# Optimization experiments

Measured on AMD Instinct MI355X. Metric: run time of the kernel, lower is better.

## Reference

```python
import jax, jax.numpy as jnp
import numpy as np

B, S_ENC, S_DEC = 4, 2048, 1024
ENC_DIM, DEC_DIM, H = 1024, 1024, 16
CROSS_DIM = max(ENC_DIM, DEC_DIM)
HEAD_DIM_DEC = DEC_DIM // H
SCALE = HEAD_DIM_DEC ** 0.5  # module divides by dec_scaling only


def _linear_params(key, d_in, d_out):
    kw, kb = jax.random.split(key)
    bound = 1.0 / np.sqrt(d_in)
    W = jax.random.uniform(kw, (d_in, d_out), jnp.float32, -bound, bound)
    b = jax.random.uniform(kb, (d_out,), jnp.float32, -bound, bound)
    return W, b


def setup_inputs() -> dict:
    key = jax.random.key(0)
    ks = jax.random.split(key, 7)
    enc = jax.random.normal(ks[0], (B, S_ENC, ENC_DIM), jnp.float32)
    dec = jax.random.normal(ks[1], (B, S_DEC, DEC_DIM), jnp.float32)
    enc_mask = jax.random.uniform(ks[2], (B, 1, 1, S_ENC)) < 0.1
    q_w, q_b = _linear_params(ks[3], DEC_DIM, CROSS_DIM)
    k_w, k_b = _linear_params(ks[4], ENC_DIM, CROSS_DIM)
    v_w, v_b = _linear_params(ks[5], ENC_DIM, DEC_DIM)
    o_w, o_b = _linear_params(ks[6], DEC_DIM, DEC_DIM)
    return {"enc": enc, "enc_mask": enc_mask, "dec": dec,
            "q_w": q_w, "q_b": q_b, "k_w": k_w, "k_b": k_b,
            "v_w": v_w, "v_b": v_b, "o_w": o_w, "o_b": o_b}


def _split_heads(x):
    b, s, d = x.shape
    return x.reshape(b, s, H, d // H).transpose(0, 2, 1, 3)  # [b,h,s,hd]


def reference(enc, enc_mask, dec, q_w, q_b, k_w, k_b, v_w, v_b, o_w, o_b):
    q = _split_heads(dec @ q_w + q_b)   # [B,H,Sq,cross_hd]
    k = _split_heads(enc @ k_w + k_b)   # [B,H,Sk,cross_hd]
    v = _split_heads(enc @ v_w + v_b)   # [B,H,Sk,dec_hd]
    logits = jnp.einsum('bhqd,bhkd->bhqk', q, k) / SCALE
    logits = jnp.where(enc_mask, -jnp.inf, logits)
    a = jax.nn.softmax(logits, axis=-1)
    x = jnp.einsum('bhqk,bhkd->bhqd', a, v)          # [B,H,Sq,dec_hd]
    x = x.transpose(0, 2, 1, 3).reshape(x.shape[0], x.shape[2], -1)  # [B,Sq,DEC_DIM]
    return x @ o_w + o_b
```

## Files before the change

kernel.cpp:

```cpp
#include <hip/hip_runtime.h>
#include <hip/hip_bf16.h>
#include <cstdint>

#define BB   4
#define SENC 2048
#define SDEC 1024
#define DM   1024
#define NH   16
#define HD   64

using short8 = __attribute__((ext_vector_type(8))) short;
using f32x4  = __attribute__((ext_vector_type(4))) float;

__device__ inline unsigned short f2bf(float f) {
    return (unsigned short)((__builtin_bit_cast(unsigned int, f) + 0x8000u) >> 16);
}
__device__ inline unsigned int pk2bf(float a, float b) {
    return ((__builtin_bit_cast(unsigned int, a) + 0x8000u) >> 16) |
           ((__builtin_bit_cast(unsigned int, b) + 0x8000u) & 0xffff0000u);
}

__device__ inline float fexp2(float x) {
#if __has_builtin(__builtin_amdgcn_exp2f)
    return __builtin_amdgcn_exp2f(x);
#else
    return exp2f(x);
#endif
}

#if __has_builtin(__builtin_amdgcn_global_load_lds)
#define HAS_GLL 1
#endif

__device__ inline void stage16(const void* g, void* l) {
#ifdef HAS_GLL
    typedef __attribute__((address_space(1))) const unsigned int guint;
    typedef __attribute__((address_space(3))) unsigned int luint;
    __builtin_amdgcn_global_load_lds((guint*)g, (luint*)l, 16, 0, 0);
#else
    *(short8*)l = *(const short8*)g;
#endif
}

__global__ __launch_bounds__(256) void cvt2_kernel(const float* __restrict__ dec,
                                                   const float* __restrict__ enc,
                                                   unsigned short* __restrict__ out) {
    const int nd = BB * SDEC * DM;
    int i = (blockIdx.x * 256 + threadIdx.x) * 4;
    const float* src = (i < nd) ? (dec + i) : (enc + (i - nd));
    float4 v = *(const float4*)src;
    ushort4 o;
    o.x = f2bf(v.x); o.y = f2bf(v.y); o.z = f2bf(v.z); o.w = f2bf(v.w);
    *(ushort4*)(out + i) = o;
}

__global__ __launch_bounds__(256) void wtrans_kernel(
    const float* __restrict__ qw, const float* __restrict__ kw,
    const float* __restrict__ vw, const float* __restrict__ ow,
    unsigned short* __restrict__ qwt, unsigned short* __restrict__ kvwt,
    unsigned short* __restrict__ owt) {
    const float* src; unsigned short* dst;
    switch (blockIdx.z) {
        case 0:  src = qw; dst = qwt; break;
        case 1:  src = kw; dst = kvwt; break;
        case 2:  src = vw; dst = kvwt + (size_t)1024 * DM; break;
        default: src = ow; dst = owt; break;
    }
    __shared__ float t[64][65];
    const int k0 = blockIdx.y * 64, n0 = blockIdx.x * 64;
    const int tid = threadIdx.x;
    #pragma unroll
    for (int it = 0; it < 16; ++it) {
        int e = it * 256 + tid, r = e >> 6, c = e & 63;
        t[r][c] = src[(size_t)(k0 + r) * DM + n0 + c];
    }
    __syncthreads();
    #pragma unroll
    for (int it = 0; it < 16; ++it) {
        int e = it * 256 + tid, r = e >> 6, c = e & 63;
        dst[(size_t)(n0 + r) * DM + k0 + c] = f2bf(t[c][r]);
    }
}

__global__ __launch_bounds__(256) void gemm_qkv_kernel(
    const unsigned short* __restrict__ encb, const unsigned short* __restrict__ decb,
    const unsigned short* __restrict__ kvwt, const unsigned short* __restrict__ qwt,
    const float* __restrict__ q_b, const float* __restrict__ k_b, const float* __restrict__ v_b,
    unsigned short* __restrict__ Qb, unsigned short* __restrict__ Kb,
    unsigned short* __restrict__ Vtb) {
    __shared__ __align__(16) unsigned short As[128 * 32];
    __shared__ __align__(16) unsigned short Bs[128 * 32];
    const int id = blockIdx.x;
    const bool isKV = id < 1024;
    const unsigned short *A, *Bt;
    int m0, n0;
    if (isKV) { A = encb; Bt = kvwt; m0 = (id >> 4) * 128; n0 = (id & 15) * 128; }
    else      { int i2 = id - 1024; A = decb; Bt = qwt; m0 = (i2 >> 3) * 128; n0 = (i2 & 7) * 128; }
    const int tid = threadIdx.x;
    const int wave = tid >> 6, lane = tid & 63, quad = lane >> 4, l16 = lane & 15;
    const int wr = wave >> 1, wc = wave & 1;
    const int r16 = lane >> 2, c8 = (lane & 3) * 8;
    f32x4 acc[4][4] = {};
    for (int kb = 0; kb < DM; kb += 32) {
        #pragma unroll
        for (int i = 0; i < 2; ++i) {
            const int row = wave * 32 + i * 16 + r16;
            stage16(&A[(size_t)(m0 + row) * DM + kb + c8], &As[row * 32 + c8]);
            stage16(&Bt[(size_t)(n0 + row) * DM + kb + c8], &Bs[row * 32 + c8]);
        }
        __syncthreads();
        short8 af[4], bfr[4];
        #pragma unroll
        for (int i = 0; i < 4; ++i) af[i] = *(const short8*)&As[(wr * 64 + i * 16 + l16) * 32 + quad * 8];
        #pragma unroll
        for (int j = 0; j < 4; ++j) bfr[j] = *(const short8*)&Bs[(wc * 64 + j * 16 + l16) * 32 + quad * 8];
        #pragma unroll
        for (int i = 0; i < 4; ++i)
            #pragma unroll
            for (int j = 0; j < 4; ++j)
                acc[i][j] = __builtin_amdgcn_mfma_f32_16x16x32_bf16(af[i], bfr[j], acc[i][j], 0, 0, 0);
        __syncthreads();
    }
    #pragma unroll
    for (int i = 0; i < 4; ++i) {
        #pragma unroll
        for (int j = 0; j < 4; ++j) {
            const int gc = n0 + wc * 64 + j * 16 + l16;
            #pragma unroll
            for (int rr = 0; rr < 4; ++rr) {
                const int gr = m0 + wr * 64 + i * 16 + quad * 4 + rr;
                if (!isKV) {
                    int b = gr >> 10, sq = gr & 1023, h = gc >> 6, d = gc & 63;
                    float v = (acc[i][j][rr] + q_b[gc]) * 0.18033688011112042f;
                    Qb[(((size_t)(b * NH + h) * SDEC + sq) << 6) + d] = f2bf(v);
                } else if (gc < 1024) {
                    int b = gr >> 11, sk = gr & 2047, h = gc >> 6, d = gc & 63;
                    Kb[(((size_t)(b * NH + h) * SENC + sk) << 6) + d] = f2bf(acc[i][j][rr] + k_b[gc]);
                } else {
                    int gc2 = gc & 1023;
                    int b = gr >> 11, sk = gr & 2047, h = gc2 >> 6, d = gc2 & 63;
                    Vtb[((size_t)(b * NH + h) * HD + d) * SENC + sk] = f2bf(acc[i][j][rr] + v_b[gc2]);
                }
            }
        }
    }
}

__global__ __launch_bounds__(256) void gemm_o_kernel(const unsigned short* __restrict__ A,
                                                     const unsigned short* __restrict__ Bt,
                                                     const float* __restrict__ bias,
                                                     float* __restrict__ Cout) {
    __shared__ __align__(16) unsigned short As[128 * 32];
    __shared__ __align__(16) unsigned short Bs[128 * 32];
    const int tid = threadIdx.x;
    const int wave = tid >> 6, lane = tid & 63, quad = lane >> 4, l16 = lane & 15;
    const int wr = wave >> 1, wc = wave & 1;
    const int m0 = blockIdx.y * 128, n0 = blockIdx.x * 128;
    const int r16 = lane >> 2, c8 = (lane & 3) * 8;
    f32x4 acc[4][4] = {};
    for (int kb = 0; kb < DM; kb += 32) {
        #pragma unroll
        for (int i = 0; i < 2; ++i) {
            const int row = wave * 32 + i * 16 + r16;
            stage16(&A[(size_t)(m0 + row) * DM + kb + c8], &As[row * 32 + c8]);
            stage16(&Bt[(size_t)(n0 + row) * DM + kb + c8], &Bs[row * 32 + c8]);
        }
        __syncthreads();
        short8 af[4], bfr[4];
        #pragma unroll
        for (int i = 0; i < 4; ++i) af[i] = *(const short8*)&As[(wr * 64 + i * 16 + l16) * 32 + quad * 8];
        #pragma unroll
        for (int j = 0; j < 4; ++j) bfr[j] = *(const short8*)&Bs[(wc * 64 + j * 16 + l16) * 32 + quad * 8];
        #pragma unroll
        for (int i = 0; i < 4; ++i)
            #pragma unroll
            for (int j = 0; j < 4; ++j)
                acc[i][j] = __builtin_amdgcn_mfma_f32_16x16x32_bf16(af[i], bfr[j], acc[i][j], 0, 0, 0);
        __syncthreads();
    }
    #pragma unroll
    for (int i = 0; i < 4; ++i)
        #pragma unroll
        for (int j = 0; j < 4; ++j) {
            const int gc = n0 + wc * 64 + j * 16 + l16;
            const float bv = bias[gc];
            #pragma unroll
            for (int rr = 0; rr < 4; ++rr) {
                const int gr = m0 + wr * 64 + i * 16 + quad * 4 + rr;
                Cout[(size_t)gr * DM + gc] = acc[i][j][rr] + bv;
            }
        }
}

__global__ __launch_bounds__(256, 2) void attn_kernel(const unsigned short* __restrict__ Qb,
                                                      const unsigned short* __restrict__ Kb,
                                                      const unsigned short* __restrict__ Vtb,
                                                      const int* __restrict__ mask,
                                                      unsigned short* __restrict__ Xb) {
    __shared__ __align__(16) unsigned short Ks[2][2][64 * 32];
    __shared__ __align__(16) unsigned short Vs[2][2][64 * 32];
    __shared__ __align__(16) unsigned short Ps[4][16 * 72];
    const int bh = blockIdx.y, b = bh >> 4, h = bh & 15;
    const int q0 = blockIdx.x * 128;
    const int tid = threadIdx.x, wave = tid >> 6, lane = tid & 63;
    const int quad = lane >> 4, l16 = lane & 15;
    const int sr = lane >> 2, sc = (lane & 3) * 8;

    const unsigned short* Kp = Kb + (size_t)bh * SENC * HD;
    const unsigned short* Vp = Vtb + (size_t)bh * HD * SENC;
    const int* mp = mask + (size_t)b * SENC;

    short8 qf[2][2];
    {
        const unsigned short* Qp = Qb + ((size_t)bh * SDEC + q0 + wave * 32) * HD;
        #pragma unroll
        for (int g = 0; g < 2; ++g) {
            qf[g][0] = *(const short8*)&Qp[(g * 16 + l16) * HD + quad * 8];
            qf[g][1] = *(const short8*)&Qp[(g * 16 + l16) * HD + 32 + quad * 8];
        }
    }

    float lsum[2] = {0.f, 0.f};
    f32x4 o[2][4] = {};

    {
        const unsigned short* kg = Kp + (size_t)(wave * 16 + sr) * HD;
        stage16(kg + sc,      &Ks[0][0][(wave * 16 + sr) * 32 + sc]);
        stage16(kg + 32 + sc, &Ks[0][1][(wave * 16 + sr) * 32 + sc]);
        const unsigned short* vg = Vp + (size_t)(wave * 16 + sr) * SENC;
        stage16(vg + sc,      &Vs[0][0][(wave * 16 + sr) * 32 + sc]);
        stage16(vg + 32 + sc, &Vs[0][1][(wave * 16 + sr) * 32 + sc]);
    }

    for (int it = 0; it < SENC / 64; ++it) {
        const int bf = it & 1;
        __syncthreads();
        if (it + 1 < SENC / 64) {
            const int nb = bf ^ 1, kb2 = (it + 1) * 64;
            const unsigned short* kg = Kp + (size_t)(kb2 + wave * 16 + sr) * HD;
            stage16(kg + sc,      &Ks[nb][0][(wave * 16 + sr) * 32 + sc]);
            stage16(kg + 32 + sc, &Ks[nb][1][(wave * 16 + sr) * 32 + sc]);
            const unsigned short* vg = Vp + (size_t)(wave * 16 + sr) * SENC + kb2;
            stage16(vg + sc,      &Vs[nb][0][(wave * 16 + sr) * 32 + sc]);
            stage16(vg + 32 + sc, &Vs[nb][1][(wave * 16 + sr) * 32 + sc]);
        }
        const int kb = it * 64;
        short8 kA0[4], kA1[4], vB0[4], vB1[4];
        #pragma unroll
        for (int j = 0; j < 4; ++j) {
            kA0[j] = *(const short8*)&Ks[bf][0][(j * 16 + l16) * 32 + quad * 8];
            kA1[j] = *(const short8*)&Ks[bf][1][(j * 16 + l16) * 32 + quad * 8];
            vB0[j] = *(const short8*)&Vs[bf][0][(j * 16 + l16) * 32 + quad * 8];
            vB1[j] = *(const short8*)&Vs[bf][1][(j * 16 + l16) * 32 + quad * 8];
        }
        int4 mi[4];
        #pragma unroll
        for (int j = 0; j < 4; ++j) mi[j] = *(const int4*)&mp[kb + j * 16 + quad * 4];
        #pragma unroll
        for (int g = 0; g < 2; ++g) {
            f32x4 st[4];
            #pragma unroll
            for (int j = 0; j < 4; ++j) {
                f32x4 z = {0.f, 0.f, 0.f, 0.f};
                z = __builtin_amdgcn_mfma_f32_16x16x32_bf16(kA0[j], qf[g][0], z, 0, 0, 0);
                st[j] = __builtin_amdgcn_mfma_f32_16x16x32_bf16(kA1[j], qf[g][1], z, 0, 0, 0);
            }
            #pragma unroll
            for (int j = 0; j < 4; ++j) {
                float p0 = mi[j].x ? 0.f : fexp2(st[j][0]);
                float p1 = mi[j].y ? 0.f : fexp2(st[j][1]);
                float p2 = mi[j].z ? 0.f : fexp2(st[j][2]);
                float p3 = mi[j].w ? 0.f : fexp2(st[j][3]);
                lsum[g] += (p0 + p1) + (p2 + p3);
                uint2 pkv;
                pkv.x = pk2bf(p0, p1);
                pkv.y = pk2bf(p2, p3);
                *(uint2*)&Ps[wave][l16 * 72 + j * 16 + quad * 4] = pkv;
            }
            asm volatile("s_waitcnt lgkmcnt(0)" ::: "memory");
            short8 pA0 = *(const short8*)&Ps[wave][l16 * 72 + quad * 8];
            short8 pA1 = *(const short8*)&Ps[wave][l16 * 72 + 32 + quad * 8];
            #pragma unroll
            for (int dj = 0; dj < 4; ++dj) {
                o[g][dj] = __builtin_amdgcn_mfma_f32_16x16x32_bf16(pA0, vB0[dj], o[g][dj], 0, 0, 0);
                o[g][dj] = __builtin_amdgcn_mfma_f32_16x16x32_bf16(pA1, vB1[dj], o[g][dj], 0, 0, 0);
            }
        }
    }
    #pragma unroll
    for (int g = 0; g < 2; ++g) {
        float lg = lsum[g];
        lg += __shfl_xor(lg, 16);
        lg += __shfl_xor(lg, 32);
        #pragma unroll
        for (int rr = 0; rr < 4; ++rr) {
            float iv = 1.0f / __shfl(lg, quad * 4 + rr, 64);
            int sq = q0 + wave * 32 + g * 16 + quad * 4 + rr;
            #pragma unroll
            for (int dj = 0; dj < 4; ++dj)
                Xb[((size_t)(b * SDEC) + sq) * DM + h * HD + dj * 16 + l16] = f2bf(o[g][dj][rr] * iv);
        }
    }
}

extern "C" void kernel_launch(void* const* d_in, const int* in_sizes, int n_in,
                              void* d_out, int out_size, void* d_ws, size_t ws_size,
                              hipStream_t stream) {
    const float* enc   = (const float*)d_in[0];
    const int*   emask = (const int*)d_in[1];
    const float* dec   = (const float*)d_in[2];
    const float* q_w   = (const float*)d_in[3];
    const float* q_b   = (const float*)d_in[4];
    const float* k_w   = (const float*)d_in[5];
    const float* k_b   = (const float*)d_in[6];
    const float* v_w   = (const float*)d_in[7];
    const float* v_b   = (const float*)d_in[8];
    const float* o_w   = (const float*)d_in[9];
    const float* o_b   = (const float*)d_in[10];
    float* out = (float*)d_out;

    char* ws = (char*)d_ws;
    unsigned short* decb = (unsigned short*)ws; ws += (size_t)4096 * 1024 * 2;
    unsigned short* encb = (unsigned short*)ws; ws += (size_t)8192 * 1024 * 2;
    unsigned short* qwt  = (unsigned short*)ws; ws += (size_t)1024 * 1024 * 2;
    unsigned short* kvwt = (unsigned short*)ws; ws += (size_t)2048 * 1024 * 2;
    unsigned short* owt  = (unsigned short*)ws; ws += (size_t)1024 * 1024 * 2;
    unsigned short* Qb   = (unsigned short*)ws; ws += (size_t)BB * NH * SDEC * HD * 2;
    unsigned short* Kb   = (unsigned short*)ws; ws += (size_t)BB * NH * SENC * HD * 2;
    unsigned short* Vtb  = (unsigned short*)ws; ws += (size_t)BB * NH * HD * SENC * 2;
    unsigned short* Xb   = (unsigned short*)ws; ws += (size_t)4096 * 1024 * 2;

    cvt2_kernel<<<12288, 256, 0, stream>>>(dec, enc, decb);
    wtrans_kernel<<<dim3(16, 16, 4), 256, 0, stream>>>(q_w, k_w, v_w, o_w, qwt, kvwt, owt);
    gemm_qkv_kernel<<<1280, 256, 0, stream>>>(encb, decb, kvwt, qwt, q_b, k_b, v_b, Qb, Kb, Vtb);
    attn_kernel<<<dim3(8, 64), 256, 0, stream>>>(Qb, Kb, Vtb, emask, Xb);
    gemm_o_kernel<<<dim3(8, 32), 256, 0, stream>>>(Xb, owt, o_b, out);
}
```

Measured before the change: 299.8 us.

## Double-buffer GEMM LDS staging, remap QKV block order, shrink output GEMM tile

Both GEMM kernels now double-buffer their LDS tiles. The next K-slice is loaded while MFMAs run on the current one, so one barrier per iteration replaces two. The QKV GEMM remaps block indices to group blocks and improve L2 reuse, hoists bias loads and writes V-transpose outputs as packed 4-element stores. The output GEMM uses 64x128 tiles with twice as many blocks for more CUs and waves, at the cost of double LDS and more redundant B-tile traffic.

New measurement: 275.9 us. 1.09x faster.

```diff
diff --git a/kernel.cpp b/kernel.cpp
--- a/kernel.cpp
+++ b/kernel.cpp
@@ -88,59 +88,90 @@
     const float* __restrict__ q_b, const float* __restrict__ k_b, const float* __restrict__ v_b,
     unsigned short* __restrict__ Qb, unsigned short* __restrict__ Kb,
     unsigned short* __restrict__ Vtb) {
-    __shared__ __align__(16) unsigned short As[128 * 32];
-    __shared__ __align__(16) unsigned short Bs[128 * 32];
+    __shared__ __align__(16) unsigned short As[2][128 * 32];
+    __shared__ __align__(16) unsigned short Bs[2][128 * 32];
     const int id = blockIdx.x;
     const bool isKV = id < 1024;
     const unsigned short *A, *Bt;
     int m0, n0;
-    if (isKV) { A = encb; Bt = kvwt; m0 = (id >> 4) * 128; n0 = (id & 15) * 128; }
-    else      { int i2 = id - 1024; A = decb; Bt = qwt; m0 = (i2 >> 3) * 128; n0 = (i2 & 7) * 128; }
+    if (isKV) {
+        const int x = id & 7, w = id >> 3;
+        A = encb; Bt = kvwt;
+        m0 = (x * 8 + (w >> 4)) * 128;
+        n0 = (w & 15) * 128;
+    } else {
+        const int i2 = id - 1024, x = i2 & 7, w = i2 >> 3;
+        A = decb; Bt = qwt;
+        m0 = (x * 4 + (w >> 3)) * 128;
+        n0 = (w & 7) * 128;
+    }
     const int tid = threadIdx.x;
     const int wave = tid >> 6, lane = tid & 63, quad = lane >> 4, l16 = lane & 15;
     const int wr = wave >> 1, wc = wave & 1;
     const int r16 = lane >> 2, c8 = (lane & 3) * 8;
     f32x4 acc[4][4] = {};
-    for (int kb = 0; kb < DM; kb += 32) {
-        #pragma unroll
-        for (int i = 0; i < 2; ++i) {
-            const int row = wave * 32 + i * 16 + r16;
-            stage16(&A[(size_t)(m0 + row) * DM + kb + c8], &As[row * 32 + c8]);
-            stage16(&Bt[(size_t)(n0 + row) * DM + kb + c8], &Bs[row * 32 + c8]);
-        }
+
+    #pragma unroll
+    for (int i = 0; i < 2; ++i) {
+        const int row = wave * 32 + i * 16 + r16;
+        stage16(&A[(size_t)(m0 + row) * DM + c8], &As[0][row * 32 + c8]);
+        stage16(&Bt[(size_t)(n0 + row) * DM + c8], &Bs[0][row * 32 + c8]);
+    }
+    for (int it = 0; it < 32; ++it) {
+        const int bf = it & 1;
         __syncthreads();
+        if (it < 31) {
+            const int kb2 = (it + 1) * 32, nb = bf ^ 1;
+            #pragma unroll
+            for (int i = 0; i < 2; ++i) {
+                const int row = wave * 32 + i * 16 + r16;
+                stage16(&A[(size_t)(m0 + row) * DM + kb2 + c8], &As[nb][row * 32 + c8]);
+                stage16(&Bt[(size_t)(n0 + row) * DM + kb2 + c8], &Bs[nb][row * 32 + c8]);
+            }
+        }
         short8 af[4], bfr[4];
         #pragma unroll
-        for (int i = 0; i < 4; ++i) af[i] = *(const short8*)&As[(wr * 64 + i * 16 + l16) * 32 + quad * 8];
-        #pragma unroll
-        for (int j = 0; j < 4; ++j) bfr[j] = *(const short8*)&Bs[(wc * 64 + j * 16 + l16) * 32 + quad * 8];
+        for (int i = 0; i < 4; ++i) af[i] = *(const short8*)&As[bf][(wr * 64 + i * 16 + l16) * 32 + quad * 8];
+        #pragma unroll
+        for (int j = 0; j < 4; ++j) bfr[j] = *(const short8*)&Bs[bf][(wc * 64 + j * 16 + l16) * 32 + quad * 8];
         #pragma unroll
         for (int i = 0; i < 4; ++i)
             #pragma unroll
             for (int j = 0; j < 4; ++j)
                 acc[i][j] = __builtin_amdgcn_mfma_f32_16x16x32_bf16(af[i], bfr[j], acc[i][j], 0, 0, 0);
-        __syncthreads();
     }
     #pragma unroll
     for (int i = 0; i < 4; ++i) {
         #pragma unroll
         for (int j = 0; j < 4; ++j) {
             const int gc = n0 + wc * 64 + j * 16 + l16;
-            #pragma unroll
-            for (int rr = 0; rr < 4; ++rr) {
-                const int gr = m0 + wr * 64 + i * 16 + quad * 4 + rr;
-                if (!isKV) {
-                    int b = gr >> 10, sq = gr & 1023, h = gc >> 6, d = gc & 63;
-                    float v = (acc[i][j][rr] + q_b[gc]) * 0.18033688011112042f;
+            const int gr0 = m0 + wr * 64 + i * 16 + quad * 4;
+            if (!isKV) {
+                const float bv = q_b[gc];
+                int h = gc >> 6, d = gc & 63;
+                #pragma unroll
+                for (int rr = 0; rr < 4; ++rr) {
+                    int gr = gr0 + rr, b = gr >> 10, sq = gr & 1023;
+                    float v = (acc[i][j][rr] + bv) * 0.18033688011112042f;
                     Qb[(((size_t)(b * NH + h) * SDEC + sq) << 6) + d] = f2bf(v);
-                } else if (gc < 1024) {
-                    int b = gr >> 11, sk = gr & 2047, h = gc >> 6, d = gc & 63;
-                    Kb[(((size_t)(b * NH + h) * SENC + sk) << 6) + d] = f2bf(acc[i][j][rr] + k_b[gc]);
-                } else {
-                    int gc2 = gc & 1023;
-                    int b = gr >> 11, sk = gr & 2047, h = gc2 >> 6, d = gc2 & 63;
-                    Vtb[((size_t)(b * NH + h) * HD + d) * SENC + sk] = f2bf(acc[i][j][rr] + v_b[gc2]);
                 }
+            } else if (gc < 1024) {
+                const float bv = k_b[gc];
+                int h = gc >> 6, d = gc & 63;
+                #pragma unroll
+                for (int rr = 0; rr < 4; ++rr) {
+                    int gr = gr0 + rr, b = gr >> 11, sk = gr & 2047;
+                    Kb[(((size_t)(b * NH + h) * SENC + sk) << 6) + d] = f2bf(acc[i][j][rr] + bv);
+                }
+            } else {
+                const int gc2 = gc & 1023;
+                const float bv = v_b[gc2];
+                int h = gc2 >> 6, d = gc2 & 63;
+                int b = gr0 >> 11, sk = gr0 & 2047;
+                uint2 pk;
+                pk.x = pk2bf(acc[i][j][0] + bv, acc[i][j][1] + bv);
+                pk.y = pk2bf(acc[i][j][2] + bv, acc[i][j][3] + bv);
+                *(uint2*)&Vtb[((size_t)(b * NH + h) * HD + d) * SENC + sk] = pk;
             }
         }
     }
@@ -150,43 +181,55 @@
                                                      const unsigned short* __restrict__ Bt,
                                                      const float* __restrict__ bias,
                                                      float* __restrict__ Cout) {
-    __shared__ __align__(16) unsigned short As[128 * 32];
-    __shared__ __align__(16) unsigned short Bs[128 * 32];
+    __shared__ __align__(16) unsigned short As[2][64 * 32];
+    __shared__ __align__(16) unsigned short Bs[2][128 * 32];
     const int tid = threadIdx.x;
     const int wave = tid >> 6, lane = tid & 63, quad = lane >> 4, l16 = lane & 15;
-    const int wr = wave >> 1, wc = wave & 1;
-    const int m0 = blockIdx.y * 128, n0 = blockIdx.x * 128;
+    const int m0 = blockIdx.y * 64, n0 = blockIdx.x * 128;
     const int r16 = lane >> 2, c8 = (lane & 3) * 8;
-    f32x4 acc[4][4] = {};
-    for (int kb = 0; kb < DM; kb += 32) {
+    f32x4 acc[4][2] = {};
+    {
+        const int rowA = wave * 16 + r16;
+        stage16(&A[(size_t)(m0 + rowA) * DM + c8], &As[0][rowA * 32 + c8]);
         #pragma unroll
         for (int i = 0; i < 2; ++i) {
             const int row = wave * 32 + i * 16 + r16;
-            stage16(&A[(size_t)(m0 + row) * DM + kb + c8], &As[row * 32 + c8]);
-            stage16(&Bt[(size_t)(n0 + row) * DM + kb + c8], &Bs[row * 32 + c8]);
-        }
+            stage16(&Bt[(size_t)(n0 + row) * DM + c8], &Bs[0][row * 32 + c8]);
+        }
+    }
+    for (int it = 0; it < 32; ++it) {
+        const int bf = it & 1;
         __syncthreads();
-        short8 af[4], bfr[4];
-        #pragma unroll
-        for (int i = 0; i < 4; ++i) af[i] = *(const short8*)&As[(wr * 64 + i * 16 + l16) * 32 + quad * 8];
-        #pragma unroll
-        for (int j = 0; j < 4; ++j) bfr[j] = *(const short8*)&Bs[(wc * 64 + j * 16 + l16) * 32 + quad * 8];
+        if (it < 31) {
+            const int kb2 = (it + 1) * 32, nb = bf ^ 1;
+            const int rowA = wave * 16 + r16;
+            stage16(&A[(size_t)(m0 + rowA) * DM + kb2 + c8], &As[nb][rowA * 32 + c8]);
+            #pragma unroll
+            for (int i = 0; i < 2; ++i) {
+                const int row = wave * 32 + i * 16 + r16;
+                stage16(&Bt[(size_t)(n0 + row) * DM + kb2 + c8], &Bs[nb][row * 32 + c8]);
+            }
+        }
+        short8 af[4], bfr[2];
+        #pragma unroll
+        for (int i = 0; i < 4; ++i) af[i] = *(const short8*)&As[bf][(i * 16 + l16) * 32 + quad * 8];
+        #pragma unroll
+        for (int j = 0; j < 2; ++j) bfr[j] = *(const short8*)&Bs[bf][(wave * 32 + j * 16 + l16) * 32 + quad * 8];
         #pragma unroll
         for (int i = 0; i < 4; ++i)
             #pragma unroll
-            for (int j = 0; j < 4; ++j)
+            for (int j = 0; j < 2; ++j)
                 acc[i][j] = __builtin_amdgcn_mfma_f32_16x16x32_bf16(af[i], bfr[j], acc[i][j], 0, 0, 0);
-        __syncthreads();
     }
     #pragma unroll
     for (int i = 0; i < 4; ++i)
         #pragma unroll
-        for (int j = 0; j < 4; ++j) {
-            const int gc = n0 + wc * 64 + j * 16 + l16;
+        for (int j = 0; j < 2; ++j) {
+            const int gc = n0 + wave * 32 + j * 16 + l16;
             const float bv = bias[gc];
             #pragma unroll
             for (int rr = 0; rr < 4; ++rr) {
-                const int gr = m0 + wr * 64 + i * 16 + quad * 4 + rr;
+                const int gr = m0 + i * 16 + quad * 4 + rr;
                 Cout[(size_t)gr * DM + gc] = acc[i][j][rr] + bv;
             }
         }
@@ -334,5 +377,5 @@
     wtrans_kernel<<<dim3(16, 16, 4), 256, 0, stream>>>(q_w, k_w, v_w, o_w, qwt, kvwt, owt);
     gemm_qkv_kernel<<<1280, 256, 0, stream>>>(encb, decb, kvwt, qwt, q_b, k_b, v_b, Qb, Kb, Vtb);
     attn_kernel<<<dim3(8, 64), 256, 0, stream>>>(Qb, Kb, Vtb, emask, Xb);
-    gemm_o_kernel<<<dim3(8, 32), 256, 0, stream>>>(Xb, owt, o_b, out);
-}
+    gemm_o_kernel<<<dim3(8, 64), 256, 0, stream>>>(Xb, owt, o_b, out);
+}
```
